# Optimization experiments

Measured on AMD Instinct MI355X. Metric: run time of the kernel, lower is better.

The kernel has to match this reference:

```python
import jax, jax.numpy as jnp
import numpy as np

INPUT_SIZE = 512
HIDDEN_SIZE = 512
FORGET_BIAS = 1.0
B, T = 256, 256


def _xavier_uniform(key, shape):
    fan_out, fan_in = shape
    bound = jnp.sqrt(6.0 / (fan_in + fan_out))
    return jax.random.uniform(key, shape, jnp.float32, -bound, bound)


def setup_inputs() -> dict:
    key = jax.random.key(0)
    k1, k2, k3 = jax.random.split(key, 3)
    H, I = HIDDEN_SIZE, INPUT_SIZE
    x = jax.random.normal(k1, (B, T, I), jnp.float32)
    h0 = jnp.zeros((1, B, H), jnp.float32)
    c0 = jnp.zeros((1, B, H), jnp.float32)
    W_ih = _xavier_uniform(k2, (4 * H, I))
    W_hh = _xavier_uniform(k3, (4 * H, H))
    # biases init to zero, then forget_bias added to [H:2H] of BOTH biases (as in source)
    b = jnp.zeros((4 * H,), jnp.float32).at[H:2 * H].add(FORGET_BIAS)
    return {"input_tensor": x, "h0": h0, "c0": c0,
            "W_ih": W_ih, "W_hh": W_hh, "b_ih": b, "b_hh": b}


def reference(input_tensor, h0, c0, W_ih, W_hh, b_ih, b_hh):
    H = HIDDEN_SIZE
    half = H // 2
    b_all = b_ih + b_hh  # [4H]
    # precompute input projections for all timesteps: [T, B, 4H]
    x_proj = jnp.einsum('bti,gi->tbg', input_tensor, W_ih) + b_all

    def step(carry, xg):
        h, c, m = carry
        gates = xg + h @ W_hh.T                      # [B, 4H]
        i, f, g, o = jnp.split(gates, 4, axis=-1)
        c = jax.nn.sigmoid(f) * c + jax.nn.sigmoid(i) * jnp.tanh(g)
        h = jax.nn.sigmoid(o) * jnp.tanh(c)
        m = jnp.maximum(m, h[:, :half])              # running max over first half
        out = jnp.concatenate([m, h[:, half:]], axis=0)  # torch.cat default dim=0 -> [2B, half]
        return (h, c, m), out

    h_init = h0[0]
    c_init = c0[0]
    m_init = jnp.full((h_init.shape[0], half), -jnp.inf, h_init.dtype)
    (h_n, c_n, _), outs = jax.lax.scan(step, (h_init, c_init, m_init), x_proj)
    all_out = jnp.transpose(outs, (1, 0, 2))         # [2B, T, half]
    return all_out, h_n[None], c_n[None]
```

## Files before the change

### kernel.cpp

```cpp
#include <hip/hip_runtime.h>
#include <cstdint>

#define B_SZ 256
#define T_SZ 256
#define I_SZ 512
#define H_SZ 512
#define HALF 256

typedef __attribute__((ext_vector_type(8))) __bf16 bf16x8;
typedef __attribute__((ext_vector_type(8))) short short8;
typedef __attribute__((ext_vector_type(4))) float f32x4;
typedef __attribute__((ext_vector_type(4))) unsigned int uint4v;

__device__ __forceinline__ unsigned short f2bf(float f) {
  unsigned int u = __float_as_uint(f);
  u = (u + 0x7FFFu + ((u >> 16) & 1u)) >> 16;
  return (unsigned short)u;
}

__device__ __forceinline__ float sigm(float x) {
  return __builtin_amdgcn_rcpf(1.f + __expf(-x));
}
__device__ __forceinline__ float tanh_(float x) {
  float ax = fabsf(x);
  float e = __expf(-2.f * ax);
  float r = (1.f - e) * __builtin_amdgcn_rcpf(1.f + e);
  return copysignf(r, x);
}

__global__ void cvt_f32_bf16(const float* __restrict__ src, unsigned short* __restrict__ dst) {
  long i = ((long)blockIdx.x * 256 + threadIdx.x) * 8;
  float4 a = *(const float4*)(src + i);
  float4 b = *(const float4*)(src + i + 4);
  unsigned int w0 = (unsigned)f2bf(a.x) | ((unsigned)f2bf(a.y) << 16);
  unsigned int w1 = (unsigned)f2bf(a.z) | ((unsigned)f2bf(a.w) << 16);
  unsigned int w2 = (unsigned)f2bf(b.x) | ((unsigned)f2bf(b.y) << 16);
  unsigned int w3 = (unsigned)f2bf(b.z) | ((unsigned)f2bf(b.w) << 16);
  uint4v v = {w0, w1, w2, w3};
  *(uint4v*)(dst + i) = v;
}

__global__ void cvt_h0_tag(const float* __restrict__ h0, unsigned long long* __restrict__ dst) {
  int i = blockIdx.x * 256 + threadIdx.x;
  unsigned int pw = (unsigned)f2bf(h0[2 * i]) | ((unsigned)f2bf(h0[2 * i + 1]) << 16);
  dst[i] = (unsigned long long)pw;
}

__global__ void pack_w(const float* __restrict__ Wih, const float* __restrict__ Whh,
                       unsigned short* __restrict__ wp, unsigned short* __restrict__ hp) {
  int id = blockIdx.x * 256 + threadIdx.x;
  int cid = id & 131071;
  const float* W = (id < 131072) ? Wih : Whh;
  unsigned short* D = (id < 131072) ? wp : hp;
  int l  = cid & 63;
  int ks = (cid >> 6) & 15;
  int nt = (cid >> 10) & 1;
  int w  = (cid >> 11) & 3;
  int hg = (cid >> 13) & 15;
  int row = w * 512 + hg * 32 + nt * 16 + (l & 15);
  int k0  = ks * 32 + (l >> 4) * 8;
  const float* src = W + (long)row * 512 + k0;
  unsigned int wd[4];
#pragma unroll
  for (int j = 0; j < 4; ++j) {
    unsigned int lo = f2bf(src[2 * j]);
    unsigned int hi = f2bf(src[2 * j + 1]);
    wd[j] = lo | (hi << 16);
  }
  uint4v v = {wd[0], wd[1], wd[2], wd[3]};
  *(uint4v*)(D + (long)cid * 8) = v;
}

template <int SCOPE>
__device__ __forceinline__ void poll_fetch(const unsigned long long* src,
                                           unsigned tag, int tid,
                                           unsigned int* hpad) {
  unsigned long long v[16];
#pragma unroll
  for (int i = 0; i < 16; ++i)
    v[i] = __hip_atomic_load(src + i * 256 + tid, __ATOMIC_RELAXED, SCOPE);
  bool redo = true;
  while (redo) {
    redo = false;
#pragma unroll
    for (int i = 0; i < 16; ++i) {
      if ((unsigned)(v[i] >> 32) != tag) {
        v[i] = __hip_atomic_load(src + i * 256 + tid, __ATOMIC_RELAXED, SCOPE);
        redo = true;
      }
    }
  }
#pragma unroll
  for (int i = 0; i < 16; ++i)
    hpad[i * 260 + tid] = (unsigned int)v[i];
}

template <int SCOPE>
__device__ __forceinline__ void st64(unsigned long long* p, unsigned long long v) {
  __hip_atomic_store(p, v, __ATOMIC_RELAXED, SCOPE);
}

__global__ __launch_bounds__(256, 1) void lstm_main(
    const unsigned short* __restrict__ xb,
    const float* __restrict__ c0,
    const float* __restrict__ b_ih, const float* __restrict__ b_hh,
    const unsigned short* __restrict__ wihp, const unsigned short* __restrict__ whhp,
    unsigned long long* __restrict__ hw64,
    unsigned long long* __restrict__ cnt64,
    float* __restrict__ out)
{
  const int tid  = threadIdx.x;
  const int lane = tid & 63;
  const int w    = tid >> 6;
  const int bg   = blockIdx.x & 15;
  const int hg   = blockIdx.x >> 4;
  const int s0   = hg * 32;
  const int q    = lane >> 4;
  const int c16  = lane & 15;

  __shared__ float glds[4 * 528];
  __shared__ unsigned int hpad[16 * 260];
  __shared__ int s_path;

  int xcd;
  asm volatile("s_getreg_b32 %0, hwreg(20, 0, 32)" : "=s"(xcd));
  xcd &= 15;
  if (tid == 0) {
    unsigned long long inc = 1ull << (8 * xcd);
    __hip_atomic_fetch_add(&cnt64[bg * 8], inc, __ATOMIC_RELAXED, __HIP_MEMORY_SCOPE_SYSTEM);
    unsigned long long m;
    do {
      __builtin_amdgcn_s_sleep(2);
      m = __hip_atomic_load(&cnt64[bg * 8], __ATOMIC_RELAXED, __HIP_MEMORY_SCOPE_SYSTEM);
    } while ((unsigned)((m * 0x0101010101010101ull) >> 56) < 16);
    s_path = (m == (16ull << (8 * xcd))) ? 1 : 0;
  }
  __syncthreads();
  const bool agent_path = (s_path != 0);

  bf16x8 wih[2][16], whh[2][16];
#pragma unroll
  for (int nt = 0; nt < 2; ++nt) {
#pragma unroll
    for (int ks = 0; ks < 16; ++ks) {
      int idc = ((hg * 4 + w) * 2 + nt) * 16 + ks;
      long off = ((long)(idc * 64 + lane)) * 8;
      wih[nt][ks] = __builtin_bit_cast(bf16x8, *(const short8*)(wihp + off));
      whh[nt][ks] = __builtin_bit_cast(bf16x8, *(const short8*)(whhp + off));
    }
  }

  const int jj  = tid & 31;
  const int bl0 = tid >> 5;
  const int bglob0 = bg * 16 + bl0;
  const int bglob1 = bglob0 + 8;
  float bias_v[4];
#pragma unroll
  for (int g = 0; g < 4; ++g)
    bias_v[g] = b_ih[g * 512 + s0 + jj] + b_hh[g * 512 + s0 + jj];
  float cst0 = c0[(long)bglob0 * H_SZ + s0 + jj];
  float cst1 = c0[(long)bglob1 * H_SZ + s0 + jj];
  float m0 = -INFINITY, m1 = -INFINITY;

  const unsigned short* xbase = xb + (long)(bg * 16 + c16) * T_SZ * I_SZ + q * 8;

#pragma unroll 1
  for (int t = 0; t < T_SZ; ++t) {
    f32x4 acc0 = {0.f, 0.f, 0.f, 0.f};
    f32x4 acc1 = {0.f, 0.f, 0.f, 0.f};

    const unsigned short* xt = xbase + (long)t * I_SZ;
#pragma unroll
    for (int ks = 0; ks < 16; ++ks) {
      bf16x8 a = __builtin_bit_cast(bf16x8, *(const short8*)(xt + ks * 32));
      acc0 = __builtin_amdgcn_mfma_f32_16x16x32_bf16(a, wih[0][ks], acc0, 0, 0, 0);
      acc1 = __builtin_amdgcn_mfma_f32_16x16x32_bf16(a, wih[1][ks], acc1, 0, 0, 0);
    }

    {
      const unsigned long long* src = hw64 + ((t + 1) & 1) * 65536 + bg * 4096;
      if (agent_path) poll_fetch<__HIP_MEMORY_SCOPE_AGENT>(src, (unsigned)t, tid, hpad);
      else            poll_fetch<__HIP_MEMORY_SCOPE_SYSTEM>(src, (unsigned)t, tid, hpad);
    }
    __syncthreads();

    const unsigned int* hrow = hpad + c16 * 260;
#pragma unroll
    for (int ks = 0; ks < 16; ++ks) {
      bf16x8 a = __builtin_bit_cast(bf16x8, *(const short8*)(hrow + ks * 16 + q * 4));
      acc0 = __builtin_amdgcn_mfma_f32_16x16x32_bf16(a, whh[0][ks], acc0, 0, 0, 0);
      acc1 = __builtin_amdgcn_mfma_f32_16x16x32_bf16(a, whh[1][ks], acc1, 0, 0, 0);
    }

#pragma unroll
    for (int r = 0; r < 4; ++r) {
      glds[w * 528 + (q * 4 + r) * 33 + c16]      = acc0[r];
      glds[w * 528 + (q * 4 + r) * 33 + 16 + c16] = acc1[r];
    }
    __syncthreads();

    float hv0, hv1;
#pragma unroll
    for (int it = 0; it < 2; ++it) {
      int b = bl0 + it * 8;
      float gi = glds[0 * 528 + b * 33 + jj] + bias_v[0];
      float gf = glds[1 * 528 + b * 33 + jj] + bias_v[1];
      float gg = glds[2 * 528 + b * 33 + jj] + bias_v[2];
      float go = glds[3 * 528 + b * 33 + jj] + bias_v[3];
      float& cs = it ? cst1 : cst0;
      cs = sigm(gf) * cs + sigm(gi) * tanh_(gg);
      float h = sigm(go) * tanh_(cs);
      if (it) hv1 = h; else hv0 = h;
    }
    {
      float po0 = __shfl_xor(hv0, 1);
      float po1 = __shfl_xor(hv1, 1);
      if (!(jj & 1)) {
        unsigned long long tagw = (unsigned long long)(t + 1) << 32;
        unsigned long long w0 = tagw | ((unsigned)f2bf(hv0) | ((unsigned)f2bf(po0) << 16));
        unsigned long long w1 = tagw | ((unsigned)f2bf(hv1) | ((unsigned)f2bf(po1) << 16));
        unsigned long long* d0 = hw64 + (t & 1) * 65536 + bg * 4096
                               + bl0 * 256 + (s0 >> 1) + (jj >> 1);
        if (agent_path) {
          st64<__HIP_MEMORY_SCOPE_AGENT>(d0, w0);
          st64<__HIP_MEMORY_SCOPE_AGENT>(d0 + 8 * 256, w1);
        } else {
          st64<__HIP_MEMORY_SCOPE_SYSTEM>(d0, w0);
          st64<__HIP_MEMORY_SCOPE_SYSTEM>(d0 + 8 * 256, w1);
        }
      }
    }

#pragma unroll
    for (int it = 0; it < 2; ++it) {
      int b   = bl0 + it * 8;
      int bgl = bg * 16 + b;
      float h = it ? hv1 : hv0;
      float& mm = it ? m1 : m0;
      if (hg < 8) {
        mm = fmaxf(mm, h);
        out[(long)bgl * (T_SZ * HALF) + t * HALF + s0 + jj] = mm;
      } else {
        out[(long)(256 + bgl) * (T_SZ * HALF) + t * HALF + (s0 - 256) + jj] = h;
      }
      if (t == T_SZ - 1) {
        float cs = it ? cst1 : cst0;
        out[33554432L + (long)bgl * H_SZ + s0 + jj] = h;
        out[33554432L + 131072L + (long)bgl * H_SZ + s0 + jj] = cs;
      }
    }
  }
}

extern "C" void kernel_launch(void* const* d_in, const int* in_sizes, int n_in,
                              void* d_out, int out_size, void* d_ws, size_t ws_size,
                              hipStream_t stream) {
  const float* x   = (const float*)d_in[0];
  const float* h0  = (const float*)d_in[1];
  const float* c0  = (const float*)d_in[2];
  const float* Wih = (const float*)d_in[3];
  const float* Whh = (const float*)d_in[4];
  const float* bih = (const float*)d_in[5];
  const float* bhh = (const float*)d_in[6];
  float* out = (float*)d_out;

  char* ws = (char*)d_ws;
  unsigned short* xb     = (unsigned short*)(ws);
  unsigned short* wihp   = (unsigned short*)(ws + 67108864);
  unsigned short* whhp   = (unsigned short*)(ws + 69206016);
  unsigned long long* hw = (unsigned long long*)(ws + 71303168);
  unsigned long long* cn = (unsigned long long*)(ws + 72351744);

  hipMemsetAsync(cn, 0, 4096, stream);
  cvt_f32_bf16<<<16384, 256, 0, stream>>>(x, xb);
  cvt_h0_tag<<<256, 256, 0, stream>>>(h0, hw + 65536);
  pack_w<<<1024, 256, 0, stream>>>(Wih, Whh, wihp, whhp);
  lstm_main<<<256, 256, 0, stream>>>(xb, c0, bih, bhh, wihp, whhp, hw, cn, out);
}
```

Measured before the change: 1.542 ms.

## Add per-wave sentinel flags, prefetch x into registers, defer output stores

Each wave now publishes a per-group step counter after writing its h slice, and consumers spin on a single 64-lane sentinel load before fetching the tagged h words. Spinning on one word should cost less than repeatedly polling all 16 tagged words. The next timestep's x is prefetched into registers during the h wait, and the output stores are deferred by one step so they overlap the barrier. The MFMA chains are split into two independent accumulators, and the memory scope is made a template parameter instead of a runtime branch. In exchange, register pressure rises from the x prefetch and the extra accumulators, and ordering relies on relaxed atomics with only compiler fences between the h stores and the sentinel store.

Measured after the change: 1.731 ms. 12.2% more time.

```diff
diff --git a/kernel.cpp b/kernel.cpp
--- a/kernel.cpp
+++ b/kernel.cpp
@@ -12,12 +12,14 @@
 typedef __attribute__((ext_vector_type(4))) float f32x4;
 typedef __attribute__((ext_vector_type(4))) unsigned int uint4v;
 
+#define LGKM_BARRIER() __asm__ __volatile__("s_waitcnt lgkmcnt(0)\ns_barrier" ::: "memory")
+#define COMPILER_FENCE() __asm__ __volatile__("" ::: "memory")
+
 __device__ __forceinline__ unsigned short f2bf(float f) {
   unsigned int u = __float_as_uint(f);
   u = (u + 0x7FFFu + ((u >> 16) & 1u)) >> 16;
   return (unsigned short)u;
 }
-
 __device__ __forceinline__ float sigm(float x) {
   return __builtin_amdgcn_rcpf(1.f + __expf(-x));
 }
@@ -72,51 +74,204 @@
 }
 
 template <int SCOPE>
-__device__ __forceinline__ void poll_fetch(const unsigned long long* src,
-                                           unsigned tag, int tid,
-                                           unsigned int* hpad) {
-  unsigned long long v[16];
-#pragma unroll
-  for (int i = 0; i < 16; ++i)
-    v[i] = __hip_atomic_load(src + i * 256 + tid, __ATOMIC_RELAXED, SCOPE);
-  bool redo = true;
-  while (redo) {
-    redo = false;
-#pragma unroll
-    for (int i = 0; i < 16; ++i) {
-      if ((unsigned)(v[i] >> 32) != tag) {
-        v[i] = __hip_atomic_load(src + i * 256 + tid, __ATOMIC_RELAXED, SCOPE);
-        redo = true;
-      }
-    }
-  }
-#pragma unroll
-  for (int i = 0; i < 16; ++i)
-    hpad[i * 260 + tid] = (unsigned int)v[i];
-}
-
+__device__ __forceinline__ unsigned long long ld64(const unsigned long long* p) {
+  return __hip_atomic_load(p, __ATOMIC_RELAXED, SCOPE);
+}
 template <int SCOPE>
-__device__ __forceinline__ void st64(unsigned long long* p, unsigned long long v) {
+__device__ __forceinline__ void st64v(unsigned long long* p, unsigned long long v) {
   __hip_atomic_store(p, v, __ATOMIC_RELAXED, SCOPE);
 }
 
-__global__ __launch_bounds__(256, 1) void lstm_main(
-    const unsigned short* __restrict__ xb,
-    const float* __restrict__ c0,
+template <int SCOPE>
+__device__ __forceinline__ void lstm_body(
+    const unsigned short* __restrict__ xb, const float* __restrict__ c0,
     const float* __restrict__ b_ih, const float* __restrict__ b_hh,
     const unsigned short* __restrict__ wihp, const unsigned short* __restrict__ whhp,
-    unsigned long long* __restrict__ hw64,
-    unsigned long long* __restrict__ cnt64,
-    float* __restrict__ out)
+    unsigned long long* __restrict__ hw64, unsigned long long* __restrict__ sent,
+    float* __restrict__ out, float* glds, unsigned int* hpad, int bg, int hg)
 {
   const int tid  = threadIdx.x;
   const int lane = tid & 63;
   const int w    = tid >> 6;
-  const int bg   = blockIdx.x & 15;
-  const int hg   = blockIdx.x >> 4;
   const int s0   = hg * 32;
   const int q    = lane >> 4;
   const int c16  = lane & 15;
+
+  bf16x8 wih[2][16], whh[2][16];
+#pragma unroll
+  for (int nt = 0; nt < 2; ++nt) {
+#pragma unroll
+    for (int ks = 0; ks < 16; ++ks) {
+      int idc = ((hg * 4 + w) * 2 + nt) * 16 + ks;
+      long off = ((long)(idc * 64 + lane)) * 8;
+      wih[nt][ks] = __builtin_bit_cast(bf16x8, *(const short8*)(wihp + off));
+      whh[nt][ks] = __builtin_bit_cast(bf16x8, *(const short8*)(whhp + off));
+    }
+  }
+
+  const int jj  = tid & 31;
+  const int bl0 = tid >> 5;
+  const int bglob0 = bg * 16 + bl0;
+  const int bglob1 = bglob0 + 8;
+  float bias_v[4];
+#pragma unroll
+  for (int g = 0; g < 4; ++g)
+    bias_v[g] = b_ih[g * 512 + s0 + jj] + b_hh[g * 512 + s0 + jj];
+  float cst0 = c0[(long)bglob0 * H_SZ + s0 + jj];
+  float cst1 = c0[(long)bglob1 * H_SZ + s0 + jj];
+  float m0 = -INFINITY, m1 = -INFINITY;
+  float h0p = 0.f, h1p = 0.f;
+
+  const unsigned short* xbase = xb + (long)(bg * 16 + c16) * T_SZ * I_SZ + q * 8;
+  unsigned long long* gsent = sent + bg * 64;
+
+  bf16x8 xreg[16];
+#pragma unroll
+  for (int ks = 0; ks < 16; ++ks)
+    xreg[ks] = __builtin_bit_cast(bf16x8, *(const short8*)(xbase + ks * 32));
+
+#pragma unroll 1
+  for (int t = 0; t < T_SZ; ++t) {
+    f32x4 a0a = {0,0,0,0}, a0b = {0,0,0,0}, a1a = {0,0,0,0}, a1b = {0,0,0,0};
+
+#pragma unroll
+    for (int ks = 0; ks < 8; ++ks) {
+      a0a = __builtin_amdgcn_mfma_f32_16x16x32_bf16(xreg[ks],   wih[0][ks],   a0a, 0, 0, 0);
+      a1a = __builtin_amdgcn_mfma_f32_16x16x32_bf16(xreg[ks],   wih[1][ks],   a1a, 0, 0, 0);
+      a0b = __builtin_amdgcn_mfma_f32_16x16x32_bf16(xreg[ks+8], wih[0][ks+8], a0b, 0, 0, 0);
+      a1b = __builtin_amdgcn_mfma_f32_16x16x32_bf16(xreg[ks+8], wih[1][ks+8], a1b, 0, 0, 0);
+    }
+
+    {
+      const unsigned long long* sp = gsent + lane;
+      unsigned long long sv = ld64<SCOPE>(sp);
+      while (sv < (unsigned long long)t) sv = ld64<SCOPE>(sp);
+    }
+    COMPILER_FENCE();
+
+    {
+      const unsigned long long* src = hw64 + ((t + 1) & 1) * 65536 + bg * 4096;
+      unsigned long long v[16];
+#pragma unroll
+      for (int i = 0; i < 16; ++i)
+        v[i] = ld64<SCOPE>(src + i * 256 + tid);
+      bool redo = true;
+      while (redo) {
+        redo = false;
+#pragma unroll
+        for (int i = 0; i < 16; ++i) {
+          if ((unsigned)(v[i] >> 32) != (unsigned)t) {
+            v[i] = ld64<SCOPE>(src + i * 256 + tid);
+            redo = true;
+          }
+        }
+      }
+#pragma unroll
+      for (int i = 0; i < 16; ++i)
+        hpad[i * 260 + tid] = (unsigned int)v[i];
+    }
+
+    {
+      const unsigned short* xn = xbase + (long)((t < T_SZ - 1) ? t + 1 : t) * I_SZ;
+#pragma unroll
+      for (int ks = 0; ks < 16; ++ks)
+        xreg[ks] = __builtin_bit_cast(bf16x8, *(const short8*)(xn + ks * 32));
+    }
+
+    if (t > 0) {
+#pragma unroll
+      for (int it = 0; it < 2; ++it) {
+        int bgl = bg * 16 + bl0 + it * 8;
+        if (hg < 8) {
+          float mm = it ? m1 : m0;
+          out[(long)bgl * (T_SZ * HALF) + (t - 1) * HALF + s0 + jj] = mm;
+        } else {
+          float hp = it ? h1p : h0p;
+          out[(long)(256 + bgl) * (T_SZ * HALF) + (t - 1) * HALF + (s0 - 256) + jj] = hp;
+        }
+      }
+    }
+
+    LGKM_BARRIER();
+
+    const unsigned int* hrow = hpad + c16 * 260;
+#pragma unroll
+    for (int ks = 0; ks < 8; ++ks) {
+      bf16x8 ha = __builtin_bit_cast(bf16x8, *(const uint4v*)(hrow + ks * 16 + q * 4));
+      bf16x8 hb = __builtin_bit_cast(bf16x8, *(const uint4v*)(hrow + (ks + 8) * 16 + q * 4));
+      a0a = __builtin_amdgcn_mfma_f32_16x16x32_bf16(ha, whh[0][ks],   a0a, 0, 0, 0);
+      a1a = __builtin_amdgcn_mfma_f32_16x16x32_bf16(ha, whh[1][ks],   a1a, 0, 0, 0);
+      a0b = __builtin_amdgcn_mfma_f32_16x16x32_bf16(hb, whh[0][ks+8], a0b, 0, 0, 0);
+      a1b = __builtin_amdgcn_mfma_f32_16x16x32_bf16(hb, whh[1][ks+8], a1b, 0, 0, 0);
+    }
+
+#pragma unroll
+    for (int r = 0; r < 4; ++r) {
+      glds[w * 528 + (q * 4 + r) * 33 + c16]      = a0a[r] + a0b[r];
+      glds[w * 528 + (q * 4 + r) * 33 + 16 + c16] = a1a[r] + a1b[r];
+    }
+    LGKM_BARRIER();
+
+    float hv0, hv1;
+#pragma unroll
+    for (int it = 0; it < 2; ++it) {
+      int b = bl0 + it * 8;
+      float gi = glds[0 * 528 + b * 33 + jj] + bias_v[0];
+      float gf = glds[1 * 528 + b * 33 + jj] + bias_v[1];
+      float gg = glds[2 * 528 + b * 33 + jj] + bias_v[2];
+      float go = glds[3 * 528 + b * 33 + jj] + bias_v[3];
+      float& cs = it ? cst1 : cst0;
+      cs = sigm(gf) * cs + sigm(gi) * tanh_(gg);
+      float h = sigm(go) * tanh_(cs);
+      if (it) hv1 = h; else hv0 = h;
+    }
+    {
+      float po0 = __shfl_xor(hv0, 1);
+      float po1 = __shfl_xor(hv1, 1);
+      if (!(jj & 1)) {
+        unsigned long long tagw = (unsigned long long)(t + 1) << 32;
+        unsigned long long w0 = tagw | ((unsigned)f2bf(hv0) | ((unsigned)f2bf(po0) << 16));
+        unsigned long long w1 = tagw | ((unsigned)f2bf(hv1) | ((unsigned)f2bf(po1) << 16));
+        unsigned long long* d0 = hw64 + (t & 1) * 65536 + bg * 4096
+                               + bl0 * 256 + hg * 16 + (jj >> 1);
+        st64v<SCOPE>(d0, w0);
+        st64v<SCOPE>(d0 + 8 * 256, w1);
+      }
+      COMPILER_FENCE();
+      if (lane == 0)
+        st64v<SCOPE>(gsent + hg * 4 + w, (unsigned long long)(t + 1));
+    }
+    m0 = fmaxf(m0, hv0);
+    m1 = fmaxf(m1, hv1);
+    h0p = hv0; h1p = hv1;
+  }
+
+#pragma unroll
+  for (int it = 0; it < 2; ++it) {
+    int bgl = bg * 16 + bl0 + it * 8;
+    float h = it ? h1p : h0p;
+    float cs = it ? cst1 : cst0;
+    if (hg < 8) {
+      float mm = it ? m1 : m0;
+      out[(long)bgl * (T_SZ * HALF) + 255 * HALF + s0 + jj] = mm;
+    } else {
+      out[(long)(256 + bgl) * (T_SZ * HALF) + 255 * HALF + (s0 - 256) + jj] = h;
+    }
+    out[33554432L + (long)bgl * H_SZ + s0 + jj] = h;
+    out[33554432L + 131072L + (long)bgl * H_SZ + s0 + jj] = cs;
+  }
+}
+
+__global__ __launch_bounds__(256, 1) void lstm_main(
+    const unsigned short* __restrict__ xb, const float* __restrict__ c0,
+    const float* __restrict__ b_ih, const float* __restrict__ b_hh,
+    const unsigned short* __restrict__ wihp, const unsigned short* __restrict__ whhp,
+    unsigned long long* __restrict__ hw64, unsigned long long* __restrict__ sent,
+    unsigned long long* __restrict__ cnt64, float* __restrict__ out)
+{
+  const int tid = threadIdx.x;
+  const int bg  = blockIdx.x & 15;
+  const int hg  = blockIdx.x >> 4;
 
   __shared__ float glds[4 * 528];
   __shared__ unsigned int hpad[16 * 260];
@@ -136,120 +291,13 @@
     s_path = (m == (16ull << (8 * xcd))) ? 1 : 0;
   }
   __syncthreads();
-  const bool agent_path = (s_path != 0);
-
-  bf16x8 wih[2][16], whh[2][16];
-#pragma unroll
-  for (int nt = 0; nt < 2; ++nt) {
-#pragma unroll
-    for (int ks = 0; ks < 16; ++ks) {
-      int idc = ((hg * 4 + w) * 2 + nt) * 16 + ks;
-      long off = ((long)(idc * 64 + lane)) * 8;
-      wih[nt][ks] = __builtin_bit_cast(bf16x8, *(const short8*)(wihp + off));
-      whh[nt][ks] = __builtin_bit_cast(bf16x8, *(const short8*)(whhp + off));
-    }
-  }
-
-  const int jj  = tid & 31;
-  const int bl0 = tid >> 5;
-  const int bglob0 = bg * 16 + bl0;
-  const int bglob1 = bglob0 + 8;
-  float bias_v[4];
-#pragma unroll
-  for (int g = 0; g < 4; ++g)
-    bias_v[g] = b_ih[g * 512 + s0 + jj] + b_hh[g * 512 + s0 + jj];
-  float cst0 = c0[(long)bglob0 * H_SZ + s0 + jj];
-  float cst1 = c0[(long)bglob1 * H_SZ + s0 + jj];
-  float m0 = -INFINITY, m1 = -INFINITY;
-
-  const unsigned short* xbase = xb + (long)(bg * 16 + c16) * T_SZ * I_SZ + q * 8;
-
-#pragma unroll 1
-  for (int t = 0; t < T_SZ; ++t) {
-    f32x4 acc0 = {0.f, 0.f, 0.f, 0.f};
-    f32x4 acc1 = {0.f, 0.f, 0.f, 0.f};
-
-    const unsigned short* xt = xbase + (long)t * I_SZ;
-#pragma unroll
-    for (int ks = 0; ks < 16; ++ks) {
-      bf16x8 a = __builtin_bit_cast(bf16x8, *(const short8*)(xt + ks * 32));
-      acc0 = __builtin_amdgcn_mfma_f32_16x16x32_bf16(a, wih[0][ks], acc0, 0, 0, 0);
-      acc1 = __builtin_amdgcn_mfma_f32_16x16x32_bf16(a, wih[1][ks], acc1, 0, 0, 0);
-    }
-
-    {
-      const unsigned long long* src = hw64 + ((t + 1) & 1) * 65536 + bg * 4096;
-      if (agent_path) poll_fetch<__HIP_MEMORY_SCOPE_AGENT>(src, (unsigned)t, tid, hpad);
-      else            poll_fetch<__HIP_MEMORY_SCOPE_SYSTEM>(src, (unsigned)t, tid, hpad);
-    }
-    __syncthreads();
-
-    const unsigned int* hrow = hpad + c16 * 260;
-#pragma unroll
-    for (int ks = 0; ks < 16; ++ks) {
-      bf16x8 a = __builtin_bit_cast(bf16x8, *(const short8*)(hrow + ks * 16 + q * 4));
-      acc0 = __builtin_amdgcn_mfma_f32_16x16x32_bf16(a, whh[0][ks], acc0, 0, 0, 0);
-      acc1 = __builtin_amdgcn_mfma_f32_16x16x32_bf16(a, whh[1][ks], acc1, 0, 0, 0);
-    }
-
-#pragma unroll
-    for (int r = 0; r < 4; ++r) {
-      glds[w * 528 + (q * 4 + r) * 33 + c16]      = acc0[r];
-      glds[w * 528 + (q * 4 + r) * 33 + 16 + c16] = acc1[r];
-    }
-    __syncthreads();
-
-    float hv0, hv1;
-#pragma unroll
-    for (int it = 0; it < 2; ++it) {
-      int b = bl0 + it * 8;
-      float gi = glds[0 * 528 + b * 33 + jj] + bias_v[0];
-      float gf = glds[1 * 528 + b * 33 + jj] + bias_v[1];
-      float gg = glds[2 * 528 + b * 33 + jj] + bias_v[2];
-      float go = glds[3 * 528 + b * 33 + jj] + bias_v[3];
-      float& cs = it ? cst1 : cst0;
-      cs = sigm(gf) * cs + sigm(gi) * tanh_(gg);
-      float h = sigm(go) * tanh_(cs);
-      if (it) hv1 = h; else hv0 = h;
-    }
-    {
-      float po0 = __shfl_xor(hv0, 1);
-      float po1 = __shfl_xor(hv1, 1);
-      if (!(jj & 1)) {
-        unsigned long long tagw = (unsigned long long)(t + 1) << 32;
-        unsigned long long w0 = tagw | ((unsigned)f2bf(hv0) | ((unsigned)f2bf(po0) << 16));
-        unsigned long long w1 = tagw | ((unsigned)f2bf(hv1) | ((unsigned)f2bf(po1) << 16));
-        unsigned long long* d0 = hw64 + (t & 1) * 65536 + bg * 4096
-                               + bl0 * 256 + (s0 >> 1) + (jj >> 1);
-        if (agent_path) {
-          st64<__HIP_MEMORY_SCOPE_AGENT>(d0, w0);
-          st64<__HIP_MEMORY_SCOPE_AGENT>(d0 + 8 * 256, w1);
-        } else {
-          st64<__HIP_MEMORY_SCOPE_SYSTEM>(d0, w0);
-          st64<__HIP_MEMORY_SCOPE_SYSTEM>(d0 + 8 * 256, w1);
-        }
-      }
-    }
-
-#pragma unroll
-    for (int it = 0; it < 2; ++it) {
-      int b   = bl0 + it * 8;
-      int bgl = bg * 16 + b;
-      float h = it ? hv1 : hv0;
-      float& mm = it ? m1 : m0;
-      if (hg < 8) {
-        mm = fmaxf(mm, h);
-        out[(long)bgl * (T_SZ * HALF) + t * HALF + s0 + jj] = mm;
-      } else {
-        out[(long)(256 + bgl) * (T_SZ * HALF) + t * HALF + (s0 - 256) + jj] = h;
-      }
-      if (t == T_SZ - 1) {
-        float cs = it ? cst1 : cst0;
-        out[33554432L + (long)bgl * H_SZ + s0 + jj] = h;
-        out[33554432L + 131072L + (long)bgl * H_SZ + s0 + jj] = cs;
-      }
-    }
-  }
+
+  if (s_path)
+    lstm_body<__HIP_MEMORY_SCOPE_AGENT>(xb, c0, b_ih, b_hh, wihp, whhp,
+                                        hw64, sent, out, glds, hpad, bg, hg);
+  else
+    lstm_body<__HIP_MEMORY_SCOPE_SYSTEM>(xb, c0, b_ih, b_hh, wihp, whhp,
+                                         hw64, sent, out, glds, hpad, bg, hg);
 }
 
 extern "C" void kernel_launch(void* const* d_in, const int* in_sizes, int n_in,
@@ -265,15 +313,16 @@
   float* out = (float*)d_out;
 
   char* ws = (char*)d_ws;
-  unsigned short* xb     = (unsigned short*)(ws);
-  unsigned short* wihp   = (unsigned short*)(ws + 67108864);
-  unsigned short* whhp   = (unsigned short*)(ws + 69206016);
-  unsigned long long* hw = (unsigned long long*)(ws + 71303168);
-  unsigned long long* cn = (unsigned long long*)(ws + 72351744);
-
-  hipMemsetAsync(cn, 0, 4096, stream);
+  unsigned short* xb       = (unsigned short*)(ws);
+  unsigned short* wihp     = (unsigned short*)(ws + 67108864);
+  unsigned short* whhp     = (unsigned short*)(ws + 69206016);
+  unsigned long long* hw   = (unsigned long long*)(ws + 71303168);
+  unsigned long long* sent = (unsigned long long*)(ws + 72351744);
+  unsigned long long* cn   = (unsigned long long*)(ws + 72359936);
+
+  hipMemsetAsync(sent, 0, 9216, stream);
   cvt_f32_bf16<<<16384, 256, 0, stream>>>(x, xb);
   cvt_h0_tag<<<256, 256, 0, stream>>>(h0, hw + 65536);
   pack_w<<<1024, 256, 0, stream>>>(Wih, Whh, wihp, whhp);
-  lstm_main<<<256, 256, 0, stream>>>(xb, c0, bih, bhh, wihp, whhp, hw, cn, out);
-}
+  lstm_main<<<256, 256, 0, stream>>>(xb, c0, bih, bhh, wihp, whhp, hw, sent, cn, out);
+}
```
